# Optimization experiments

Measured on AMD Instinct MI355X. Metric: run time of the kernel, lower is better.

The kernel has to match this reference:

```python
import jax, jax.numpy as jnp
import numpy as np

H = 512      # hidden_size
E = 300      # embedding_dim (word2vec)
V = 30000    # vocab size
C = 3        # num_classes
TP = 64      # premise max len
TH = 64      # hypothesis max len
B = 128      # batch


def setup_inputs() -> dict:
    key = jax.random.key(0)
    ks = jax.random.split(key, 20)
    def nrm(k, shape, scale=0.05):
        return jax.random.normal(k, shape, jnp.float32) * scale
    embed = nrm(ks[0], (V, E), 1.0).at[0].set(0.0)  # padding_idx=0 row zeroed
    return dict(
        premise=jax.random.randint(ks[1], (TP, B), 0, V),
        premise_len=jax.random.randint(ks[2], (B,), 1, TP),
        hypothesis=jax.random.randint(ks[3], (TH, B), 0, V),
        hypothesis_len=jax.random.randint(ks[4], (B,), 1, TH),
        embed=embed,
        w_e=jax.random.uniform(ks[5], (H,), jnp.float32),
        Ws=nrm(ks[6], (H, H)), Wt=nrm(ks[7], (H, H)), Wm=nrm(ks[8], (H, H)),
        Wih_p=nrm(ks[9], (4 * H, E)), bih_p=nrm(ks[10], (4 * H,)), bhh_p=nrm(ks[11], (4 * H,)),
        Wih_h=nrm(ks[12], (4 * H, E)), bih_h=nrm(ks[13], (4 * H,)), bhh_h=nrm(ks[14], (4 * H,)),
        Wih_m=nrm(ks[15], (4 * H, 2 * H)), bih_m=nrm(ks[16], (4 * H,)), bhh_m=nrm(ks[17], (4 * H,)),
        fc_w=nrm(ks[18], (C, H)), fc_b=nrm(ks[19], (C,)),
    )


def lstm_zero_state(x, Wih, bih, bhh):
    # PyTorch LSTMCell called with hx=None -> (h,c)=0, so weight_hh*h vanishes;
    # only bias_hh survives. Gate order: i, f, g, o.
    g = x @ Wih.T + bih + bhh
    i, f, gg, o = jnp.split(g, 4, axis=-1)
    c = jax.nn.sigmoid(i) * jnp.tanh(gg)
    return jax.nn.sigmoid(o) * jnp.tanh(c)


def reference(premise, premise_len, hypothesis, hypothesis_len, embed,
              w_e, Ws, Wt, Wm,
              Wih_p, bih_p, bhh_p,
              Wih_h, bih_h, bhh_h,
              Wih_m, bih_m, bhh_m,
              fc_w, fc_b):
    # Premise/hypothesis encoders: each timestep uses zero initial state (faithful).
    h_s = lstm_zero_state(embed[premise], Wih_p, bih_p, bhh_p)      # [TP, B, H]
    h_t = lstm_zero_state(embed[hypothesis], Wih_h, bih_h, bhh_h)   # [TH, B, H]
    pre_s = h_s @ Ws.T                                              # [TP, B, H]
    pre_t = h_t @ Wt.T                                              # [TH, B, H]

    def step(h_m_prev, xs):
        pt_k, ht_k = xs                                             # [B,H], [B,H]
        # additive attention: e[j,b] = w_e . tanh(Ws h_s + Wt h_t_k + Wm h_m_prev)
        scores = jnp.einsum('tbh,h->tb', jnp.tanh(pre_s + pt_k + h_m_prev @ Wm.T), w_e)
        alpha = jax.nn.softmax(scores, axis=0)                      # softmax over premise
        a_k = jnp.einsum('tb,tbh->bh', alpha, h_s)                  # [B, H]
        m_k = jnp.concatenate([a_k, ht_k], axis=1)                  # [B, 2H]
        h_m = lstm_zero_state(m_k, Wih_m, bih_m, bhh_m)             # match cell, zero state
        return h_m, None

    h0 = jnp.zeros((premise.shape[1], Ws.shape[0]), jnp.float32)
    h_m_final, _ = jax.lax.scan(step, h0, (pre_t, h_t))
    return h_m_final @ fc_w.T + fc_b                                # [B, C]
```

## Files before the change

### kernel.cpp

```cpp
#include <hip/hip_runtime.h>


#define DEV static __device__ __forceinline__

DEV float fast_sigmoid(float x) { return 1.0f / (1.0f + __expf(-x)); }
DEV float fast_tanh(float x)    { return 1.0f - 2.0f / (__expf(2.0f * x) + 1.0f); }

DEV unsigned f2bf(float x) {
    unsigned v = __float_as_uint(x);
    return (v + 0x7FFFu + ((v >> 16) & 1u)) >> 16;
}
DEV float blo(unsigned u) { return __uint_as_float(u << 16); }

DEV float ntload(const float* p) { return __builtin_nontemporal_load(p); }

typedef __attribute__((ext_vector_type(8))) short bfrag;
typedef __attribute__((ext_vector_type(4))) float ffrag;

#define G3_BLK_S 99328

DEV void cvt_hilo(const float* v, bfrag& hi, bfrag& lo)
{
#pragma unroll
    for (int z = 0; z < 8; ++z) {
        unsigned h = f2bf(v[z]);
        hi[z] = (short)h;
        lo[z] = (short)f2bf(v[z] - __uint_as_float(h << 16));
    }
}

__global__ __launch_bounds__(128, 2) void gather_fused_kernel(
    const float* __restrict__ embed, const int* __restrict__ gidx,
    const float* __restrict__ Wih,
    const float* __restrict__ bih, const float* __restrict__ bhh,
    unsigned short* __restrict__ RhB)
{
    const int wv   = threadIdx.x >> 6;
    const int lane = threadIdx.x & 63;
    const int row  = lane & 15;
    const int quad = lane >> 4;
    const int m0 = blockIdx.x * 32 + wv * 16;
    const int j0 = blockIdx.y * 64;

    const int arow = gidx[m0 + row];

    ffrag acc[3][4];
#pragma unroll
    for (int g = 0; g < 3; ++g)
#pragma unroll
        for (int n = 0; n < 4; ++n)
#pragma unroll
            for (int r = 0; r < 4; ++r) acc[g][n][r] = 0.0f;

#pragma unroll 1
    for (int k0 = 0; k0 < 300; k0 += 32) {
        const bool tail = (k0 + 32 > 300);
        float av[8];
        if (!tail) {
            const float* ap = embed + (size_t)arow * 300 + k0 + quad * 8;
            float4 aA = *(const float4*)ap;
            float4 aB = *(const float4*)(ap + 4);
            av[0]=aA.x; av[1]=aA.y; av[2]=aA.z; av[3]=aA.w;
            av[4]=aB.x; av[5]=aB.y; av[6]=aB.z; av[7]=aB.w;
        } else {
#pragma unroll
            for (int z = 0; z < 8; ++z) {
                int kk = k0 + quad * 8 + z;
                av[z] = (kk < 300) ? embed[(size_t)arow * 300 + kk] : 0.0f;
            }
        }
        bfrag ahi, alo;
        cvt_hilo(av, ahi, alo);
#pragma unroll
        for (int g = 0; g < 3; ++g) {
            const int gbase = (g == 0) ? 0 : (g == 1 ? 1024 : 1536);
#pragma unroll
            for (int n = 0; n < 4; ++n) {
                const int wrow = gbase + j0 + n * 16 + row;
                float wvv[8];
                if (!tail) {
                    const float* wp = Wih + (size_t)wrow * 300 + k0 + quad * 8;
                    float4 wA = *(const float4*)wp;
                    float4 wB = *(const float4*)(wp + 4);
                    wvv[0]=wA.x; wvv[1]=wA.y; wvv[2]=wA.z; wvv[3]=wA.w;
                    wvv[4]=wB.x; wvv[5]=wB.y; wvv[6]=wB.z; wvv[7]=wB.w;
                } else {
#pragma unroll
                    for (int z = 0; z < 8; ++z) {
                        int kk = k0 + quad * 8 + z;
                        wvv[z] = (kk < 300) ? Wih[(size_t)wrow * 300 + kk] : 0.0f;
                    }
                }
                bfrag whi, wlo;
                cvt_hilo(wvv, whi, wlo);
                acc[g][n] = __builtin_amdgcn_mfma_f32_16x16x32_bf16(ahi, whi, acc[g][n], 0, 0, 0);
                acc[g][n] = __builtin_amdgcn_mfma_f32_16x16x32_bf16(alo, whi, acc[g][n], 0, 0, 0);
                acc[g][n] = __builtin_amdgcn_mfma_f32_16x16x32_bf16(ahi, wlo, acc[g][n], 0, 0, 0);
            }
        }
    }

#pragma unroll
    for (int n = 0; n < 4; ++n) {
        const int j = j0 + n * 16 + row;
        const float b0 = bih[j]        + bhh[j];
        const float b1 = bih[1024 + j] + bhh[1024 + j];
        const float b2 = bih[1536 + j] + bhh[1536 + j];
        const int kc     = j >> 5;
        const int lane_g = ((j >> 3) & 3) * 16;
        const int z      = j & 7;
#pragma unroll
        for (int r = 0; r < 4; ++r) {
            const int m = m0 + quad * 4 + r;
            float gi = acc[0][n][r] + b0;
            float gg = acc[1][n][r] + b1;
            float go = acc[2][n][r] + b2;
            float cc = fast_sigmoid(gi) * fast_tanh(gg);
            float hv = fast_sigmoid(go) * fast_tanh(cc);
            size_t idx = ((size_t)(kc * 256 + (m >> 4)) * 64
                          + lane_g + (m & 15)) * 16 + z;
            unsigned hb = f2bf(hv);
            RhB[idx]     = (unsigned short)hb;
            RhB[idx + 8] = (unsigned short)f2bf(hv - blo(hb));
        }
    }
}

template<int HYP>
__global__ __launch_bounds__(128, 2) void fusedA_kernel(
    const uint4* __restrict__ AB,
    const float* __restrict__ Wnt,
    const float* __restrict__ Wg3,
    const float* __restrict__ bias1, const float* __restrict__ bias2,
    float* __restrict__ outNT,
    unsigned short* __restrict__ G3s, int mbase,
    float* __restrict__ outMH)
{
    const int wv   = threadIdx.x >> 6;
    const int lane = threadIdx.x & 63;
    const int row  = lane & 15;
    const int quad = lane >> 4;
    const int m0   = blockIdx.x * 128 + wv * 64;
    const int mt0  = m0 >> 4;
    const int yy   = blockIdx.y;
    const bool isNT = (yy < 8);

    int gate = 0, j0 = 0, gbase = 0, wbase, ldw;
    const float* W;
    if (isNT) {
        W = Wnt; ldw = 512; wbase = yy * 64;
    } else {
        gate = (yy - 8) >> 3;
        j0   = ((yy - 8) & 7) * 64;
        gbase = (gate == 0) ? 0 : (gate == 1 ? 1024 : 1536);
        W = Wg3; ldw = 1024; wbase = gbase + j0;
    }

    ffrag acc[4][4];
#pragma unroll
    for (int mt = 0; mt < 4; ++mt)
#pragma unroll
        for (int n = 0; n < 4; ++n)
#pragma unroll
            for (int r = 0; r < 4; ++r) acc[mt][n][r] = 0.0f;

#pragma unroll 1
    for (int k0 = 0; k0 < 512; k0 += 32) {
        const int kc = k0 >> 5;
        bfrag ahi[4], alo[4];
#pragma unroll
        for (int mt = 0; mt < 4; ++mt) {
            const uint4* ap = AB + ((size_t)(kc * 256 + mt0 + mt) * 64 + lane) * 2;
            ahi[mt] = *(const bfrag*)(ap);
            alo[mt] = *(const bfrag*)(ap + 1);
        }
#pragma unroll
        for (int n = 0; n < 4; ++n) {
            const int wrow = wbase + n * 16 + row;
            const float* wp = W + (size_t)wrow * ldw + k0 + quad * 8;
            float4 wA = *(const float4*)wp;
            float4 wB = *(const float4*)(wp + 4);
            float wvv[8] = {wA.x, wA.y, wA.z, wA.w, wB.x, wB.y, wB.z, wB.w};
            bfrag whi, wlo;
            cvt_hilo(wvv, whi, wlo);
#pragma unroll
            for (int mt = 0; mt < 4; ++mt) {
                acc[mt][n] = __builtin_amdgcn_mfma_f32_16x16x32_bf16(ahi[mt], whi, acc[mt][n], 0, 0, 0);
                acc[mt][n] = __builtin_amdgcn_mfma_f32_16x16x32_bf16(alo[mt], whi, acc[mt][n], 0, 0, 0);
                acc[mt][n] = __builtin_amdgcn_mfma_f32_16x16x32_bf16(ahi[mt], wlo, acc[mt][n], 0, 0, 0);
            }
        }
    }

    if (isNT) {
#pragma unroll
        for (int mt = 0; mt < 4; ++mt)
#pragma unroll
            for (int n = 0; n < 4; ++n)
#pragma unroll
                for (int r = 0; r < 4; ++r)
                    outNT[(size_t)(m0 + mt * 16 + quad * 4 + r) * 512
                          + wbase + n * 16 + row] = acc[mt][n][r];
    } else if (!HYP) {
#pragma unroll
        for (int n = 0; n < 4; ++n) {
            const int j = j0 + n * 16 + row;
#pragma unroll
            for (int mt = 0; mt < 4; ++mt)
#pragma unroll
                for (int r = 0; r < 4; ++r) {
                    const int mg = mbase + m0 + mt * 16 + quad * 4 + r;
                    const int t = mg >> 7, b = mg & 127;
                    size_t idx = (size_t)b * G3_BLK_S
                               + ((size_t)(gate * 512 + j)) * 64 + t;
                    G3s[idx] = (unsigned short)f2bf(acc[mt][n][r]);
                }
        }
    } else {
#pragma unroll
        for (int n = 0; n < 4; ++n) {
            const int j = j0 + n * 16 + row;
            const float bb = bias1[gbase + j] + bias2[gbase + j];
#pragma unroll
            for (int mt = 0; mt < 4; ++mt)
#pragma unroll
                for (int r = 0; r < 4; ++r) {
                    const int m = m0 + mt * 16 + quad * 4 + r;
                    outMH[((size_t)m * 3 + gate) * 512 + j] = acc[mt][n][r] + bb;
                }
        }
    }
}

__global__ __launch_bounds__(256) void pack_wm_kernel(
    const float* __restrict__ Wm, unsigned* __restrict__ WmB)
{
    int i = blockIdx.x * 256 + threadIdx.x;
    int u = i & 3, lane = (i >> 2) & 63;
    int nt = (i >> 8) & 31, kc = i >> 13;
    int row = nt * 16 + (lane & 15);
    int k = kc * 32 + ((lane >> 4) << 3) + u * 2;
    unsigned lo = f2bf(Wm[(size_t)row * 512 + k]);
    unsigned hi = f2bf(Wm[(size_t)row * 512 + k + 1]);
    WmB[i] = lo | (hi << 16);
}

__global__ __launch_bounds__(1024) void phaseB_kernel(
    const float* __restrict__ pre_s, const float* __restrict__ pre_t,
    const float* __restrict__ pre_m_h,
    const unsigned* __restrict__ WmB, const unsigned short* __restrict__ G3s,
    const float* __restrict__ w_e,
    const float* __restrict__ fc_w,  const float* __restrict__ fc_b,
    float* __restrict__ out)
{
    extern __shared__ __align__(16) float psL[];
    __shared__ __align__(16) float hm[512];
    __shared__ __align__(16) float base[512];
    __shared__ __align__(16) float wesh[512];
    __shared__ __align__(16) float sc[64];
    __shared__ __align__(16) float red[2 * 512];
    __shared__ __align__(16) float gates3[1536];
    __shared__ __align__(16) unsigned short hmh[512];
    __shared__ __align__(16) unsigned short hml[512];
    __shared__ __align__(16) unsigned short sch[64];
    __shared__ __align__(16) unsigned short scl[64];

    const int b    = blockIdx.x;
    const int tid  = threadIdx.x;
    const int wv   = tid >> 6;
    const int lane = tid & 63;
    const int col  = lane & 15;
    const int quad = lane >> 4;

    if (tid < 512) {
        wesh[tid] = w_e[tid];
        hm[tid] = 0.0f; hmh[tid] = 0; hml[tid] = 0;
    }
    for (int i = tid; i < 32768; i += 1024) {
        int t = i >> 9, h = i & 511;
        psL[i] = ntload(&pre_s[((size_t)t * 128 + b) * 512 + h]);
    }
    __syncthreads();

    for (int k = 0; k < 64; ++k) {
        {
            const int kh2 = wv >> 3;
            const int tp  = (wv & 7) * 4;
            ffrag a0 = {0.0f,0.0f,0.0f,0.0f}, a1 = {0.0f,0.0f,0.0f,0.0f};
            ffrag a2 = {0.0f,0.0f,0.0f,0.0f}, a3 = {0.0f,0.0f,0.0f,0.0f};
            const uint4* wp = (const uint4*)WmB
                            + ((size_t)(kh2 * 8) * 32 + tp) * 64 + lane;
            const unsigned short* ab = ((lane & 8) == 0) ? hmh : hml;
#pragma unroll 1
            for (int kc = 0; kc < 8; ++kc) {
                bfrag a  = *(const bfrag*)&ab[(kh2 * 8 + kc) * 32 + quad * 8];
                bfrag w0 = *(const bfrag*)(wp);
                bfrag w1 = *(const bfrag*)(wp + 64);
                bfrag w2 = *(const bfrag*)(wp + 128);
                bfrag w3 = *(const bfrag*)(wp + 192);
                a0 = __builtin_amdgcn_mfma_f32_16x16x32_bf16(a, w0, a0, 0, 0, 0);
                a1 = __builtin_amdgcn_mfma_f32_16x16x32_bf16(a, w1, a1, 0, 0, 0);
                a2 = __builtin_amdgcn_mfma_f32_16x16x32_bf16(a, w2, a2, 0, 0, 0);
                a3 = __builtin_amdgcn_mfma_f32_16x16x32_bf16(a, w3, a3, 0, 0, 0);
                wp += 2048;
            }
            float s0 = a0[0] + __shfl_xor(a0[0], 32);
            float s1 = a1[0] + __shfl_xor(a1[0], 32);
            float s2 = a2[0] + __shfl_xor(a2[0], 32);
            float s3 = a3[0] + __shfl_xor(a3[0], 32);
            if (lane < 16) {
                float* rr = &red[kh2 * 512];
                rr[(tp + 0) * 16 + lane] = s0;
                rr[(tp + 1) * 16 + lane] = s1;
                rr[(tp + 2) * 16 + lane] = s2;
                rr[(tp + 3) * 16 + lane] = s3;
            }
        }
        __syncthreads();
        if (tid < 512)
            base[tid] = red[tid] + red[512 + tid]
                      + ntload(&pre_t[((size_t)k * 128 + b) * 512 + tid]);
        __syncthreads();

#pragma unroll
        for (int tt = 0; tt < 4; ++tt) {
            int t = wv * 4 + tt;
            const float* ps = &psL[t * 512];
            float p = 0.0f;
#pragma unroll
            for (int u = 0; u < 8; ++u) {
                int h = lane + 64 * u;
                p += wesh[h] * fast_tanh(ps[h] + base[h]);
            }
#pragma unroll
            for (int off = 32; off; off >>= 1) p += __shfl_xor(p, off);
            if (lane == 0) sc[t] = p;
        }
        __syncthreads();

        if (wv == 0) {
            float s = sc[lane], mx = s;
#pragma unroll
            for (int off = 32; off; off >>= 1) mx = fmaxf(mx, __shfl_xor(mx, off));
            float e = __expf(s - mx), sum = e;
#pragma unroll
            for (int off = 32; off; off >>= 1) sum += __shfl_xor(sum, off);
            float a = e / sum;
            unsigned hb = f2bf(a);
            sch[lane] = (unsigned short)hb;
            scl[lane] = (unsigned short)f2bf(a - blo(hb));
        }
        __syncthreads();

        {
            const unsigned short* ab = ((lane & 8) == 0) ? sch : scl;
            bfrag aA = *(const bfrag*)&ab[quad * 8];
            bfrag aB = *(const bfrag*)&ab[32 + quad * 8];
            const unsigned short* gp = G3s + (size_t)b * G3_BLK_S
                                     + ((size_t)(wv * 96) + col) * 64 + quad * 8;
            ffrag g[6];
#pragma unroll
            for (int t6 = 0; t6 < 6; ++t6) {
                g[t6][0] = 0.0f; g[t6][1] = 0.0f; g[t6][2] = 0.0f; g[t6][3] = 0.0f;
            }
#pragma unroll
            for (int t6 = 0; t6 < 6; ++t6) {
                bfrag w0 = *(const bfrag*)(gp + t6 * 1024);
                g[t6] = __builtin_amdgcn_mfma_f32_16x16x32_bf16(aA, w0, g[t6], 0, 0, 0);
            }
#pragma unroll
            for (int t6 = 0; t6 < 6; ++t6) {
                bfrag w1 = *(const bfrag*)(gp + t6 * 1024 + 32);
                g[t6] = __builtin_amdgcn_mfma_f32_16x16x32_bf16(aB, w1, g[t6], 0, 0, 0);
            }
#pragma unroll
            for (int t6 = 0; t6 < 6; ++t6) {
                float s = g[t6][0] + __shfl_xor(g[t6][0], 32);
                if (lane < 16) gates3[(wv * 6 + t6) * 16 + lane] = s;
            }
        }
        __syncthreads();

        if (tid < 512) {
            const size_t m = (size_t)k * 128 + b;
            float gi = gates3[tid]        + ntload(&pre_m_h[(m * 3 + 0) * 512 + tid]);
            float gg = gates3[512 + tid]  + ntload(&pre_m_h[(m * 3 + 1) * 512 + tid]);
            float go = gates3[1024 + tid] + ntload(&pre_m_h[(m * 3 + 2) * 512 + tid]);
            float cc = fast_sigmoid(gi) * fast_tanh(gg);
            float hv = fast_sigmoid(go) * fast_tanh(cc);
            hm[tid] = hv;
            unsigned hb = f2bf(hv);
            hmh[tid] = (unsigned short)hb;
            hml[tid] = (unsigned short)f2bf(hv - blo(hb));
        }
        __syncthreads();
    }

    if (wv < 3) {
        float p = 0.0f;
#pragma unroll
        for (int u = 0; u < 8; ++u) {
            int h = lane + 64 * u;
            p += hm[h] * fc_w[wv * 512 + h];
        }
#pragma unroll
        for (int off = 32; off; off >>= 1) p += __shfl_xor(p, off);
        if (lane == 0) out[b * 3 + wv] = p + fc_b[wv];
    }
}

extern "C" void kernel_launch(void* const* d_in, const int* in_sizes, int n_in,
                              void* d_out, int out_size, void* d_ws, size_t ws_size,
                              hipStream_t stream)
{
    (void)in_sizes; (void)n_in; (void)out_size;
    const int*   premise    = (const int*)d_in[0];
    const int*   hypothesis = (const int*)d_in[2];
    const float* embed  = (const float*)d_in[4];
    const float* w_e    = (const float*)d_in[5];
    const float* Ws     = (const float*)d_in[6];
    const float* Wt     = (const float*)d_in[7];
    const float* Wm     = (const float*)d_in[8];
    const float* Wih_p  = (const float*)d_in[9];
    const float* bih_p  = (const float*)d_in[10];
    const float* bhh_p  = (const float*)d_in[11];
    const float* Wih_h  = (const float*)d_in[12];
    const float* bih_h  = (const float*)d_in[13];
    const float* bhh_h  = (const float*)d_in[14];
    const float* Wih_m  = (const float*)d_in[15];
    const float* bih_m  = (const float*)d_in[16];
    const float* bhh_m  = (const float*)d_in[17];
    const float* fc_w   = (const float*)d_in[18];
    const float* fc_b   = (const float*)d_in[19];

    float* ws      = (float*)d_ws;
    unsigned short* RhB = (unsigned short*)ws;
    const uint4* RhB4   = (const uint4*)ws;
    float* pre_s   = ws + 2097152;
    float* pre_t   = ws + 6291456;
    float* pre_m_h = ws + 10485760;
    unsigned short* G3s = (unsigned short*)(ws + 23068672);
    unsigned* WmB  = (unsigned*)ws;
    float* outp    = (float*)d_out;
    if (ws_size < (size_t)29556736 * 4) return;

    dim3 blk2(128);
    dim3 blk(256);

    for (int h = 0; h < 2; ++h) {
        gather_fused_kernel<<<dim3(128, 8), blk2, 0, stream>>>(
            embed, premise + h * 4096, Wih_p, bih_p, bhh_p, RhB);
        fusedA_kernel<0><<<dim3(32, 32), blk2, 0, stream>>>(
            RhB4, Ws, Wih_m, nullptr, nullptr,
            pre_s + (size_t)h * 2097152, G3s, h * 4096, nullptr);
    }
    for (int h = 0; h < 2; ++h) {
        gather_fused_kernel<<<dim3(128, 8), blk2, 0, stream>>>(
            embed, hypothesis + h * 4096, Wih_h, bih_h, bhh_h, RhB);
        fusedA_kernel<1><<<dim3(32, 32), blk2, 0, stream>>>(
            RhB4, Wt, Wih_m + 512, bih_m, bhh_m,
            pre_t + (size_t)h * 2097152, nullptr, 0,
            pre_m_h + (size_t)h * 6291456);
    }

    pack_wm_kernel<<<512, blk, 0, stream>>>(Wm, WmB);

    static int attr_done = 0;
    if (!attr_done) {
        hipFuncSetAttribute((const void*)phaseB_kernel,
                            hipFuncAttributeMaxDynamicSharedMemorySize, 131072);
        attr_done = 1;
    }
    phaseB_kernel<<<dim3(128), dim3(1024), 131072, stream>>>(
        pre_s, pre_t, pre_m_h, WmB, G3s, w_e, fc_w, fc_b, outp);
}
```

Measured before the change: 1.316 ms.

## Prepack weight fragments to bf16 hi/lo MFMA layout once before GEMMs

Adds a kernel that converts Wt and Wih_m into prepacked bf16 hi/lo MFMA fragment layouts, so the hypothesis and premise GEMM kernels load fragments directly instead of converting fp32 weights inside the inner loop. Packed weights live temporarily in the pre_s workspace region, which forces the hypothesis pass to run first. The premise pass is split into a separate G3 kernel and an NT kernel, and the NT kernel still converts Ws on the fly because its output overwrites the pre_s buffer holding the packed weights. This costs one extra pack kernel launch and some workspace aliasing.

```diff
diff --git a/kernel.cpp b/kernel.cpp
--- a/kernel.cpp
+++ b/kernel.cpp
@@ -27,6 +27,36 @@
         hi[z] = (short)h;
         lo[z] = (short)f2bf(v[z] - __uint_as_float(h << 16));
     }
+}
+
+__global__ __launch_bounds__(256) void pack_wfrag_kernel(
+    const float* __restrict__ Wt, const float* __restrict__ Wm3,
+    uint4* __restrict__ WtP, uint4* __restrict__ W3aP, uint4* __restrict__ W3hP)
+{
+    const int bid = blockIdx.x;
+    int i, NT, coff, ldw;
+    const float* W;
+    uint4* dst;
+    if (bid < 128)      { i = bid * 256 + threadIdx.x;         NT = 32; W = Wt;  dst = WtP;  coff = 0;   ldw = 512;  }
+    else if (bid < 512) { i = (bid - 128) * 256 + threadIdx.x; NT = 96; W = Wm3; dst = W3aP; coff = 0;   ldw = 1024; }
+    else                { i = (bid - 512) * 256 + threadIdx.x; NT = 96; W = Wm3; dst = W3hP; coff = 512; ldw = 1024; }
+
+    const int lane = i & 63;
+    const int nt   = (i >> 6) % NT;
+    const int kc   = (i >> 6) / NT;
+    const int srow = nt * 16 + (lane & 15);
+    int row = srow;
+    if (NT == 96) {
+        int gate = srow >> 9;
+        row = (gate == 0 ? 0 : (gate == 1 ? 1024 : 1536)) + (srow & 511);
+    }
+    const int k = kc * 32 + ((lane >> 4) << 3) + coff;
+    const float* wp = W + (size_t)row * ldw + k;
+    float wvv[8] = {wp[0], wp[1], wp[2], wp[3], wp[4], wp[5], wp[6], wp[7]};
+    bfrag whi, wlo;
+    cvt_hilo(wvv, whi, wlo);
+    *(bfrag*)(dst + (size_t)i * 2)     = whi;
+    *(bfrag*)(dst + (size_t)i * 2 + 1) = wlo;
 }
 
 __global__ __launch_bounds__(128, 2) void gather_fused_kernel(
@@ -126,15 +156,11 @@
     }
 }
 
-template<int HYP>
-__global__ __launch_bounds__(128, 2) void fusedA_kernel(
+__global__ __launch_bounds__(128, 2) void fusedA1_kernel(
     const uint4* __restrict__ AB,
-    const float* __restrict__ Wnt,
-    const float* __restrict__ Wg3,
+    const uint4* __restrict__ WtP, const uint4* __restrict__ W3hP,
     const float* __restrict__ bias1, const float* __restrict__ bias2,
-    float* __restrict__ outNT,
-    unsigned short* __restrict__ G3s, int mbase,
-    float* __restrict__ outMH)
+    float* __restrict__ outNT, float* __restrict__ outMH)
 {
     const int wv   = threadIdx.x >> 6;
     const int lane = threadIdx.x & 63;
@@ -145,15 +171,14 @@
     const int yy   = blockIdx.y;
     const bool isNT = (yy < 8);
 
-    int gate = 0, j0 = 0, gbase = 0, wbase, ldw;
-    const float* W;
-    if (isNT) {
-        W = Wnt; ldw = 512; wbase = yy * 64;
-    } else {
-        gate = (yy - 8) >> 3;
-        j0   = ((yy - 8) & 7) * 64;
+    int gate = 0, j0 = 0, gbase = 0, NTs, ntb;
+    const uint4* WP;
+    if (isNT) { WP = WtP; NTs = 32; ntb = yy * 4; }
+    else {
+        gate  = (yy - 8) >> 3;
+        j0    = ((yy - 8) & 7) * 64;
         gbase = (gate == 0) ? 0 : (gate == 1 ? 1024 : 1536);
-        W = Wg3; ldw = 1024; wbase = gbase + j0;
+        WP = W3hP; NTs = 96; ntb = gate * 32 + ((yy - 8) & 7) * 4;
     }
 
     ffrag acc[4][4];
@@ -176,8 +201,137 @@
         }
 #pragma unroll
         for (int n = 0; n < 4; ++n) {
-            const int wrow = wbase + n * 16 + row;
-            const float* wp = W + (size_t)wrow * ldw + k0 + quad * 8;
+            const uint4* wf = WP + ((size_t)(kc * NTs + ntb + n) * 64 + lane) * 2;
+            bfrag whi = *(const bfrag*)(wf);
+            bfrag wlo = *(const bfrag*)(wf + 1);
+#pragma unroll
+            for (int mt = 0; mt < 4; ++mt) {
+                acc[mt][n] = __builtin_amdgcn_mfma_f32_16x16x32_bf16(ahi[mt], whi, acc[mt][n], 0, 0, 0);
+                acc[mt][n] = __builtin_amdgcn_mfma_f32_16x16x32_bf16(alo[mt], whi, acc[mt][n], 0, 0, 0);
+                acc[mt][n] = __builtin_amdgcn_mfma_f32_16x16x32_bf16(ahi[mt], wlo, acc[mt][n], 0, 0, 0);
+            }
+        }
+    }
+
+    if (isNT) {
+#pragma unroll
+        for (int mt = 0; mt < 4; ++mt)
+#pragma unroll
+            for (int n = 0; n < 4; ++n)
+#pragma unroll
+                for (int r = 0; r < 4; ++r)
+                    outNT[(size_t)(m0 + mt * 16 + quad * 4 + r) * 512
+                          + yy * 64 + n * 16 + row] = acc[mt][n][r];
+    } else {
+#pragma unroll
+        for (int n = 0; n < 4; ++n) {
+            const int j = j0 + n * 16 + row;
+            const float bb = bias1[gbase + j] + bias2[gbase + j];
+#pragma unroll
+            for (int mt = 0; mt < 4; ++mt)
+#pragma unroll
+                for (int r = 0; r < 4; ++r) {
+                    const int m = m0 + mt * 16 + quad * 4 + r;
+                    outMH[((size_t)m * 3 + gate) * 512 + j] = acc[mt][n][r] + bb;
+                }
+        }
+    }
+}
+
+__global__ __launch_bounds__(128, 2) void g3pack_pw_kernel(
+    const uint4* __restrict__ AB, const uint4* __restrict__ W3aP,
+    unsigned short* __restrict__ G3s, int mbase)
+{
+    const int wv   = threadIdx.x >> 6;
+    const int lane = threadIdx.x & 63;
+    const int row  = lane & 15;
+    const int quad = lane >> 4;
+    const int m0   = blockIdx.x * 128 + wv * 64;
+    const int mt0  = m0 >> 4;
+    const int gate = blockIdx.y >> 3;
+    const int j0   = (blockIdx.y & 7) * 64;
+    const int ntb  = gate * 32 + (blockIdx.y & 7) * 4;
+
+    ffrag acc[4][4];
+#pragma unroll
+    for (int mt = 0; mt < 4; ++mt)
+#pragma unroll
+        for (int n = 0; n < 4; ++n)
+#pragma unroll
+            for (int r = 0; r < 4; ++r) acc[mt][n][r] = 0.0f;
+
+#pragma unroll 1
+    for (int k0 = 0; k0 < 512; k0 += 32) {
+        const int kc = k0 >> 5;
+        bfrag ahi[4], alo[4];
+#pragma unroll
+        for (int mt = 0; mt < 4; ++mt) {
+            const uint4* ap = AB + ((size_t)(kc * 256 + mt0 + mt) * 64 + lane) * 2;
+            ahi[mt] = *(const bfrag*)(ap);
+            alo[mt] = *(const bfrag*)(ap + 1);
+        }
+#pragma unroll
+        for (int n = 0; n < 4; ++n) {
+            const uint4* wf = W3aP + ((size_t)(kc * 96 + ntb + n) * 64 + lane) * 2;
+            bfrag whi = *(const bfrag*)(wf);
+            bfrag wlo = *(const bfrag*)(wf + 1);
+#pragma unroll
+            for (int mt = 0; mt < 4; ++mt) {
+                acc[mt][n] = __builtin_amdgcn_mfma_f32_16x16x32_bf16(ahi[mt], whi, acc[mt][n], 0, 0, 0);
+                acc[mt][n] = __builtin_amdgcn_mfma_f32_16x16x32_bf16(alo[mt], whi, acc[mt][n], 0, 0, 0);
+                acc[mt][n] = __builtin_amdgcn_mfma_f32_16x16x32_bf16(ahi[mt], wlo, acc[mt][n], 0, 0, 0);
+            }
+        }
+    }
+#pragma unroll
+    for (int n = 0; n < 4; ++n) {
+        const int j = j0 + n * 16 + row;
+#pragma unroll
+        for (int mt = 0; mt < 4; ++mt)
+#pragma unroll
+            for (int r = 0; r < 4; ++r) {
+                const int mg = mbase + m0 + mt * 16 + quad * 4 + r;
+                const int t = mg >> 7, b = mg & 127;
+                size_t idx = (size_t)b * G3_BLK_S
+                           + ((size_t)(gate * 512 + j)) * 64 + t;
+                G3s[idx] = (unsigned short)f2bf(acc[mt][n][r]);
+            }
+    }
+}
+
+__global__ __launch_bounds__(128, 2) void mfma_nt_kernel(
+    const uint4* __restrict__ AB, const float* __restrict__ W,
+    float* __restrict__ C)
+{
+    const int wv   = threadIdx.x >> 6;
+    const int lane = threadIdx.x & 63;
+    const int row  = lane & 15;
+    const int quad = lane >> 4;
+    const int m0 = blockIdx.x * 128 + wv * 64;
+    const int n0 = blockIdx.y * 64;
+    const int mt0 = m0 >> 4;
+
+    ffrag acc[4][4];
+#pragma unroll
+    for (int mt = 0; mt < 4; ++mt)
+#pragma unroll
+        for (int n = 0; n < 4; ++n)
+#pragma unroll
+            for (int r = 0; r < 4; ++r) acc[mt][n][r] = 0.0f;
+
+#pragma unroll 1
+    for (int k0 = 0; k0 < 512; k0 += 32) {
+        const int kc = k0 >> 5;
+        bfrag ahi[4], alo[4];
+#pragma unroll
+        for (int mt = 0; mt < 4; ++mt) {
+            const uint4* ap = AB + ((size_t)(kc * 256 + mt0 + mt) * 64 + lane) * 2;
+            ahi[mt] = *(const bfrag*)(ap);
+            alo[mt] = *(const bfrag*)(ap + 1);
+        }
+#pragma unroll
+        for (int n = 0; n < 4; ++n) {
+            const float* wp = W + (size_t)(n0 + n * 16 + row) * 512 + k0 + quad * 8;
             float4 wA = *(const float4*)wp;
             float4 wB = *(const float4*)(wp + 4);
             float wvv[8] = {wA.x, wA.y, wA.z, wA.w, wB.x, wB.y, wB.z, wB.w};
@@ -191,45 +345,14 @@
             }
         }
     }
-
-    if (isNT) {
-#pragma unroll
-        for (int mt = 0; mt < 4; ++mt)
-#pragma unroll
-            for (int n = 0; n < 4; ++n)
-#pragma unroll
-                for (int r = 0; r < 4; ++r)
-                    outNT[(size_t)(m0 + mt * 16 + quad * 4 + r) * 512
-                          + wbase + n * 16 + row] = acc[mt][n][r];
-    } else if (!HYP) {
-#pragma unroll
-        for (int n = 0; n < 4; ++n) {
-            const int j = j0 + n * 16 + row;
-#pragma unroll
-            for (int mt = 0; mt < 4; ++mt)
-#pragma unroll
-                for (int r = 0; r < 4; ++r) {
-                    const int mg = mbase + m0 + mt * 16 + quad * 4 + r;
-                    const int t = mg >> 7, b = mg & 127;
-                    size_t idx = (size_t)b * G3_BLK_S
-                               + ((size_t)(gate * 512 + j)) * 64 + t;
-                    G3s[idx] = (unsigned short)f2bf(acc[mt][n][r]);
-                }
-        }
-    } else {
-#pragma unroll
-        for (int n = 0; n < 4; ++n) {
-            const int j = j0 + n * 16 + row;
-            const float bb = bias1[gbase + j] + bias2[gbase + j];
-#pragma unroll
-            for (int mt = 0; mt < 4; ++mt)
-#pragma unroll
-                for (int r = 0; r < 4; ++r) {
-                    const int m = m0 + mt * 16 + quad * 4 + r;
-                    outMH[((size_t)m * 3 + gate) * 512 + j] = acc[mt][n][r] + bb;
-                }
-        }
-    }
+#pragma unroll
+    for (int mt = 0; mt < 4; ++mt)
+#pragma unroll
+        for (int n = 0; n < 4; ++n)
+#pragma unroll
+            for (int r = 0; r < 4; ++r)
+                C[(size_t)(m0 + mt * 16 + quad * 4 + r) * 512 + n0 + n * 16 + row]
+                    = acc[mt][n][r];
 }
 
 __global__ __launch_bounds__(256) void pack_wm_kernel(
@@ -441,26 +564,31 @@
     float* pre_m_h = ws + 10485760;
     unsigned short* G3s = (unsigned short*)(ws + 23068672);
     unsigned* WmB  = (unsigned*)ws;
+    uint4* WtP  = (uint4*)(pre_s);
+    uint4* W3hP = (uint4*)(pre_s + 262144);
+    uint4* W3aP = (uint4*)(pre_s + 3407872);
     float* outp    = (float*)d_out;
     if (ws_size < (size_t)29556736 * 4) return;
 
     dim3 blk2(128);
     dim3 blk(256);
 
+    pack_wfrag_kernel<<<896, blk, 0, stream>>>(Wt, Wih_m, WtP, W3aP, W3hP);
+
+    for (int h = 0; h < 2; ++h) {
+        gather_fused_kernel<<<dim3(128, 8), blk2, 0, stream>>>(
+            embed, hypothesis + h * 4096, Wih_h, bih_h, bhh_h, RhB);
+        fusedA1_kernel<<<dim3(32, 32), blk2, 0, stream>>>(
+            RhB4, WtP, W3hP, bih_m, bhh_m,
+            pre_t + (size_t)h * 2097152, pre_m_h + (size_t)h * 6291456);
+    }
     for (int h = 0; h < 2; ++h) {
         gather_fused_kernel<<<dim3(128, 8), blk2, 0, stream>>>(
             embed, premise + h * 4096, Wih_p, bih_p, bhh_p, RhB);
-        fusedA_kernel<0><<<dim3(32, 32), blk2, 0, stream>>>(
-            RhB4, Ws, Wih_m, nullptr, nullptr,
-            pre_s + (size_t)h * 2097152, G3s, h * 4096, nullptr);
-    }
-    for (int h = 0; h < 2; ++h) {
-        gather_fused_kernel<<<dim3(128, 8), blk2, 0, stream>>>(
-            embed, hypothesis + h * 4096, Wih_h, bih_h, bhh_h, RhB);
-        fusedA_kernel<1><<<dim3(32, 32), blk2, 0, stream>>>(
-            RhB4, Wt, Wih_m + 512, bih_m, bhh_m,
-            pre_t + (size_t)h * 2097152, nullptr, 0,
-            pre_m_h + (size_t)h * 6291456);
+        g3pack_pw_kernel<<<dim3(32, 24), blk2, 0, stream>>>(
+            RhB4, W3aP, G3s, h * 4096);
+        mfma_nt_kernel<<<dim3(32, 8), blk2, 0, stream>>>(
+            RhB4, Ws, pre_s + (size_t)h * 2097152);
     }
 
     pack_wm_kernel<<<512, blk, 0, stream>>>(Wm, WmB);
```

New measurement: 1.367 ms. 1.04x slower.
